# Kernel optimization log

Measured on AMD Instinct MI355X. Metric: run time of the kernel, lower is better.

The kernel has to match this reference:

```python
import jax, jax.numpy as jnp
import numpy as np

NTYPE = 4
ALPHA = 0.2  # LeakyReLU negative slope
N_NODES = 65536
N_FEAT = 64
N_HEADS = 4
BATCH = 131072


def setup_inputs() -> dict:
    key = jax.random.key(0)
    k1, k2, k3 = jax.random.split(key, 3)
    total = BATCH * NTYPE  # 524288 = 8 * N_NODES -> guarantees full node coverage
    ids = jnp.tile(jnp.arange(N_NODES, dtype=jnp.int64 if jax.config.jax_enable_x64 else jnp.int32), total // N_NODES)
    batch = jax.random.permutation(k1, ids).reshape(BATCH, NTYPE)
    batch_features = jax.random.normal(k2, (N_NODES, N_FEAT), dtype=jnp.float32)
    att_weights = jax.random.normal(k3, (N_HEADS, NTYPE - 1), dtype=jnp.float32) * 0.1
    return {"batch": batch, "batch_features": batch_features, "att_weights": att_weights}


def reference(batch, batch_features, att_weights):
    ntype = NTYPE
    B = batch.shape[0]
    N, F = batch_features.shape
    # filters = ~eye(ntype): for row i, keep all columns except i
    cols = np.stack([[j for j in range(ntype) if j != i] for i in range(ntype)])  # [ntype, ntype-1]
    # neighbor indices per (filter i, batch row b): batch[b, cols[i]]
    neigh = jnp.transpose(batch[:, cols], (1, 0, 2)).reshape(ntype * B, ntype - 1)  # [ntype*B, ntype-1]
    feat = batch_features[neigh]  # gather: [ntype*B, ntype-1, F]
    # att_feat = att_weights @ feat (broadcast matmul): [ntype*B, a, F]
    att_feat = jnp.einsum('ak,rkf->raf', att_weights, feat)
    # target node of each feat row: batch.T.flatten()
    batch_nodes = batch.T.reshape(-1)  # [ntype*B]
    # max-pool rows per node (nodes = 0..N-1 by construction): [N, a, F]
    agg = jax.ops.segment_max(att_feat, batch_nodes, num_segments=N)
    agg = jnp.transpose(agg, (1, 0, 2))  # [a, N, F]
    out = batch_features[None, :, :] + agg  # broadcast add: [a, N, F]
    out = jnp.transpose(out, (1, 0, 2))  # [N, a, F]
    out = jax.nn.leaky_relu(out, negative_slope=ALPHA)
    return out.reshape(N, -1)  # concat=True -> [N, a*F]
```

## Files before the change

### kernel.cpp

```cpp
#include <hip/hip_runtime.h>

#define N_NODES 65536
#define N_FEAT  64
#define N_HEADS 4
#define BATCHSZ 131072
#define NTYPE   4
#define ALPHA   0.2f
#define SRC_PER_NODE 8

__global__ __launch_bounds__(256) void build_index(const int* __restrict__ batch,
                                                   int* __restrict__ cnt,
                                                   int* __restrict__ idx) {
    int b = blockIdx.x * blockDim.x + threadIdx.x;
    int4 br = ((const int4*)batch)[b];
    int t0 = br.x, t1 = br.y, t2 = br.z, t3 = br.w;
    int p0 = atomicAdd(&cnt[t0], 1);
    int p1 = atomicAdd(&cnt[t1], 1);
    int p2 = atomicAdd(&cnt[t2], 1);
    int p3 = atomicAdd(&cnt[t3], 1);
    idx[t0 * SRC_PER_NODE + p0] = b * 4 + 0;
    idx[t1 * SRC_PER_NODE + p1] = b * 4 + 1;
    idx[t2 * SRC_PER_NODE + p2] = b * 4 + 2;
    idx[t3 * SRC_PER_NODE + p3] = b * 4 + 3;
}


__device__ __forceinline__ float4 f4max(float4 a, float4 b) {
    return make_float4(fmaxf(a.x, b.x), fmaxf(a.y, b.y), fmaxf(a.z, b.z), fmaxf(a.w, b.w));
}
__device__ __forceinline__ float4 f4shflx(float4 v, int m) {
    return make_float4(__shfl_xor(v.x, m), __shfl_xor(v.y, m), __shfl_xor(v.z, m), __shfl_xor(v.w, m));
}
__device__ __forceinline__ float4 f4mix(float w0, float w1, float w2, float4 a, float4 b, float4 c) {
    return make_float4(fmaf(w0, a.x, fmaf(w1, b.x, w2 * c.x)),
                       fmaf(w0, a.y, fmaf(w1, b.y, w2 * c.y)),
                       fmaf(w0, a.z, fmaf(w1, b.z, w2 * c.z)),
                       fmaf(w0, a.w, fmaf(w1, b.w, w2 * c.w)));
}

__global__ __launch_bounds__(256) void gat_agg(const int* __restrict__ batch,
                                               const float* __restrict__ feat,
                                               const float* __restrict__ att,
                                               const int* __restrict__ idx,
                                               float* __restrict__ out) {
    const int wave = threadIdx.x >> 6;
    const int lane = threadIdx.x & 63;
    const int q    = lane >> 4;
    const int fl   = lane & 15;
    const int t = blockIdx.x * 4 + wave;

    float w[N_HEADS][3];
    #pragma unroll
    for (int a = 0; a < N_HEADS; ++a)
        #pragma unroll
        for (int k = 0; k < 3; ++k)
            w[a][k] = att[a * 3 + k];

    const int4* batch4 = (const int4*)batch;

    const int4* ip = (const int4*)(idx + t * SRC_PER_NODE);
    int4 s01 = ip[0];
    int4 s23 = ip[1];
    int uA = (q < 2) ? ((q == 0) ? s01.x : s01.z) : ((q == 2) ? s23.x : s23.z);
    int uB = (q < 2) ? ((q == 0) ? s01.y : s01.w) : ((q == 2) ? s23.y : s23.w);

    float4 m0 = make_float4(-INFINITY, -INFINITY, -INFINITY, -INFINITY);
    float4 m1 = m0, m2 = m0, m3 = m0;

    #define DO_SRC(U) {                                                          \
        int b_ = (U) >> 2;                                                       \
        int i_ = (U) & 3;                                                        \
        int4 br = batch4[b_];                                                    \
        int n0 = (i_ == 0) ? br.y : br.x;                                        \
        int n1 = (i_ <= 1) ? br.z : br.y;                                        \
        int n2 = (i_ <= 2) ? br.w : br.z;                                        \
        float4 f0 = *(const float4*)(feat + n0 * N_FEAT + 4 * fl);               \
        float4 f1 = *(const float4*)(feat + n1 * N_FEAT + 4 * fl);               \
        float4 f2 = *(const float4*)(feat + n2 * N_FEAT + 4 * fl);               \
        m0 = f4max(m0, f4mix(w[0][0], w[0][1], w[0][2], f0, f1, f2));            \
        m1 = f4max(m1, f4mix(w[1][0], w[1][1], w[1][2], f0, f1, f2));            \
        m2 = f4max(m2, f4mix(w[2][0], w[2][1], w[2][2], f0, f1, f2));            \
        m3 = f4max(m3, f4mix(w[3][0], w[3][1], w[3][2], f0, f1, f2));            \
    }

    DO_SRC(uA);
    DO_SRC(uB);
    #undef DO_SRC

    m0 = f4max(m0, f4shflx(m0, 16));  m0 = f4max(m0, f4shflx(m0, 32));
    m1 = f4max(m1, f4shflx(m1, 16));  m1 = f4max(m1, f4shflx(m1, 32));
    m2 = f4max(m2, f4shflx(m2, 16));  m2 = f4max(m2, f4shflx(m2, 32));
    m3 = f4max(m3, f4shflx(m3, 16));  m3 = f4max(m3, f4shflx(m3, 32));

    float4 sel = (q < 2) ? ((q == 0) ? m0 : m1) : ((q == 2) ? m2 : m3);
    float4 ft = *(const float4*)(feat + t * N_FEAT + 4 * fl);
    float4 o = make_float4(ft.x + sel.x, ft.y + sel.y, ft.z + sel.z, ft.w + sel.w);
    o.x = fmaxf(o.x, ALPHA * o.x);
    o.y = fmaxf(o.y, ALPHA * o.y);
    o.z = fmaxf(o.z, ALPHA * o.z);
    o.w = fmaxf(o.w, ALPHA * o.w);
    *(float4*)(out + t * (N_HEADS * N_FEAT) + 4 * lane) = o;
}

extern "C" void kernel_launch(void* const* d_in, const int* in_sizes, int n_in,
                              void* d_out, int out_size, void* d_ws, size_t ws_size,
                              hipStream_t stream) {
    const int*   batch = (const int*)d_in[0];
    const float* feat  = (const float*)d_in[1];
    const float* att   = (const float*)d_in[2];
    float* out = (float*)d_out;

    int* cnt = (int*)d_ws;
    int* idx = cnt + N_NODES;

    hipMemsetAsync(cnt, 0, N_NODES * sizeof(int), stream);
    build_index<<<BATCHSZ / 256, 256, 0, stream>>>(batch, cnt, idx);
    gat_agg<<<N_NODES / 4, 256, 0, stream>>>(batch, feat, att, idx, out);
}
```

Measured before the change: 165.4 us.

## Gather fp16 features with pre-resolved neighbor ids, nontemporal output stores

Adds a pass that converts the feature table to fp16 and gathers neighbor features in half precision, halving gather bytes. The index build now stores the three neighbor node ids packed into 16-bit fields, which removes the dependent batch-row lookup in the aggregation kernel. Output stores become nontemporal to avoid polluting cache. This costs an extra kernel launch, adds precision loss in the weighted max, and relies on node ids fitting in 16 bits.

```diff
diff --git a/kernel.cpp b/kernel.cpp
--- a/kernel.cpp
+++ b/kernel.cpp
@@ -1,4 +1,5 @@
 #include <hip/hip_runtime.h>
+#include <hip/hip_fp16.h>
 
 #define N_NODES 65536
 #define N_FEAT  64
@@ -8,20 +9,38 @@
 #define ALPHA   0.2f
 #define SRC_PER_NODE 8
 
+typedef float f32x4 __attribute__((ext_vector_type(4)));
+
+__global__ __launch_bounds__(256) void to_half(const float* __restrict__ feat,
+                                               __half* __restrict__ feat_h) {
+    int i = (blockIdx.x * 256 + threadIdx.x) * 8;
+    float4 a = *(const float4*)(feat + i);
+    float4 b = *(const float4*)(feat + i + 4);
+    __half2 h0 = __floats2half2_rn(a.x, a.y);
+    __half2 h1 = __floats2half2_rn(a.z, a.w);
+    __half2 h2 = __floats2half2_rn(b.x, b.y);
+    __half2 h3 = __floats2half2_rn(b.z, b.w);
+    uint4 o;
+    o.x = __builtin_bit_cast(unsigned int, h0);
+    o.y = __builtin_bit_cast(unsigned int, h1);
+    o.z = __builtin_bit_cast(unsigned int, h2);
+    o.w = __builtin_bit_cast(unsigned int, h3);
+    *(uint4*)(feat_h + i) = o;
+}
+
 __global__ __launch_bounds__(256) void build_index(const int* __restrict__ batch,
                                                    int* __restrict__ cnt,
-                                                   int* __restrict__ idx) {
+                                                   int2* __restrict__ idx2) {
     int b = blockIdx.x * blockDim.x + threadIdx.x;
     int4 br = ((const int4*)batch)[b];
-    int t0 = br.x, t1 = br.y, t2 = br.z, t3 = br.w;
-    int p0 = atomicAdd(&cnt[t0], 1);
-    int p1 = atomicAdd(&cnt[t1], 1);
-    int p2 = atomicAdd(&cnt[t2], 1);
-    int p3 = atomicAdd(&cnt[t3], 1);
-    idx[t0 * SRC_PER_NODE + p0] = b * 4 + 0;
-    idx[t1 * SRC_PER_NODE + p1] = b * 4 + 1;
-    idx[t2 * SRC_PER_NODE + p2] = b * 4 + 2;
-    idx[t3 * SRC_PER_NODE + p3] = b * 4 + 3;
+    int p0 = atomicAdd(&cnt[br.x], 1);
+    int p1 = atomicAdd(&cnt[br.y], 1);
+    int p2 = atomicAdd(&cnt[br.z], 1);
+    int p3 = atomicAdd(&cnt[br.w], 1);
+    if (p0 < SRC_PER_NODE) idx2[br.x * SRC_PER_NODE + p0] = make_int2(br.y | (br.z << 16), br.w);
+    if (p1 < SRC_PER_NODE) idx2[br.y * SRC_PER_NODE + p1] = make_int2(br.x | (br.z << 16), br.w);
+    if (p2 < SRC_PER_NODE) idx2[br.z * SRC_PER_NODE + p2] = make_int2(br.x | (br.y << 16), br.w);
+    if (p3 < SRC_PER_NODE) idx2[br.w * SRC_PER_NODE + p3] = make_int2(br.x | (br.y << 16), br.z);
 }
 
 
@@ -37,11 +56,17 @@
                        fmaf(w0, a.z, fmaf(w1, b.z, w2 * c.z)),
                        fmaf(w0, a.w, fmaf(w1, b.w, w2 * c.w)));
 }
+__device__ __forceinline__ float4 loadh4(const __half* p) {
+    uint2 r = *(const uint2*)p;
+    float2 f01 = __half22float2(__builtin_bit_cast(__half2, r.x));
+    float2 f23 = __half22float2(__builtin_bit_cast(__half2, r.y));
+    return make_float4(f01.x, f01.y, f23.x, f23.y);
+}
 
-__global__ __launch_bounds__(256) void gat_agg(const int* __restrict__ batch,
-                                               const float* __restrict__ feat,
+__global__ __launch_bounds__(256) void gat_agg(const float* __restrict__ feat,
+                                               const __half* __restrict__ feat_h,
                                                const float* __restrict__ att,
-                                               const int* __restrict__ idx,
+                                               const int2* __restrict__ idx2,
                                                float* __restrict__ out) {
     const int wave = threadIdx.x >> 6;
     const int lane = threadIdx.x & 63;
@@ -56,35 +81,25 @@
         for (int k = 0; k < 3; ++k)
             w[a][k] = att[a * 3 + k];
 
-    const int4* batch4 = (const int4*)batch;
-
-    const int4* ip = (const int4*)(idx + t * SRC_PER_NODE);
-    int4 s01 = ip[0];
-    int4 s23 = ip[1];
-    int uA = (q < 2) ? ((q == 0) ? s01.x : s01.z) : ((q == 2) ? s23.x : s23.z);
-    int uB = (q < 2) ? ((q == 0) ? s01.y : s01.w) : ((q == 2) ? s23.y : s23.w);
+    int4 s = ((const int4*)(idx2 + t * SRC_PER_NODE))[q];
+    int a0 = s.x & 0xffff, a1 = ((unsigned)s.x) >> 16, a2 = s.y & 0xffff;
+    int b0 = s.z & 0xffff, b1 = ((unsigned)s.z) >> 16, b2 = s.w & 0xffff;
 
     float4 m0 = make_float4(-INFINITY, -INFINITY, -INFINITY, -INFINITY);
     float4 m1 = m0, m2 = m0, m3 = m0;
 
-    #define DO_SRC(U) {                                                          \
-        int b_ = (U) >> 2;                                                       \
-        int i_ = (U) & 3;                                                        \
-        int4 br = batch4[b_];                                                    \
-        int n0 = (i_ == 0) ? br.y : br.x;                                        \
-        int n1 = (i_ <= 1) ? br.z : br.y;                                        \
-        int n2 = (i_ <= 2) ? br.w : br.z;                                        \
-        float4 f0 = *(const float4*)(feat + n0 * N_FEAT + 4 * fl);               \
-        float4 f1 = *(const float4*)(feat + n1 * N_FEAT + 4 * fl);               \
-        float4 f2 = *(const float4*)(feat + n2 * N_FEAT + 4 * fl);               \
+    #define DO_SRC(N0, N1, N2) {                                                 \
+        float4 f0 = loadh4(feat_h + (N0) * N_FEAT + 4 * fl);                     \
+        float4 f1 = loadh4(feat_h + (N1) * N_FEAT + 4 * fl);                     \
+        float4 f2 = loadh4(feat_h + (N2) * N_FEAT + 4 * fl);                     \
         m0 = f4max(m0, f4mix(w[0][0], w[0][1], w[0][2], f0, f1, f2));            \
         m1 = f4max(m1, f4mix(w[1][0], w[1][1], w[1][2], f0, f1, f2));            \
         m2 = f4max(m2, f4mix(w[2][0], w[2][1], w[2][2], f0, f1, f2));            \
         m3 = f4max(m3, f4mix(w[3][0], w[3][1], w[3][2], f0, f1, f2));            \
     }
 
-    DO_SRC(uA);
-    DO_SRC(uB);
+    DO_SRC(a0, a1, a2);
+    DO_SRC(b0, b1, b2);
     #undef DO_SRC
 
     m0 = f4max(m0, f4shflx(m0, 16));  m0 = f4max(m0, f4shflx(m0, 32));
@@ -99,7 +114,8 @@
     o.y = fmaxf(o.y, ALPHA * o.y);
     o.z = fmaxf(o.z, ALPHA * o.z);
     o.w = fmaxf(o.w, ALPHA * o.w);
-    *(float4*)(out + t * (N_HEADS * N_FEAT) + 4 * lane) = o;
+    f32x4 ov = {o.x, o.y, o.z, o.w};
+    __builtin_nontemporal_store(ov, (f32x4*)(out + t * (N_HEADS * N_FEAT) + 4 * lane));
 }
 
 extern "C" void kernel_launch(void* const* d_in, const int* in_sizes, int n_in,
@@ -110,10 +126,14 @@
     const float* att   = (const float*)d_in[2];
     float* out = (float*)d_out;
 
-    int* cnt = (int*)d_ws;
-    int* idx = cnt + N_NODES;
+    char* ws = (char*)d_ws;
+    int*    cnt    = (int*)ws;
+    int2*   idx2   = (int2*)(ws + N_NODES * sizeof(int));
+    __half* feat_h = (__half*)(ws + N_NODES * sizeof(int)
+                                  + N_NODES * SRC_PER_NODE * sizeof(int2));
 
     hipMemsetAsync(cnt, 0, N_NODES * sizeof(int), stream);
-    build_index<<<BATCHSZ / 256, 256, 0, stream>>>(batch, cnt, idx);
-    gat_agg<<<N_NODES / 4, 256, 0, stream>>>(batch, feat, att, idx, out);
+    to_half<<<(N_NODES * N_FEAT) / (256 * 8), 256, 0, stream>>>(feat, feat_h);
+    build_index<<<BATCHSZ / 256, 256, 0, stream>>>(batch, cnt, idx2);
+    gat_agg<<<N_NODES / 4, 256, 0, stream>>>(feat, feat_h, att, idx2, out);
 }
```

Result: faster. 140.4 us (-15.1%).
